# Optimization experiments

Hardware: AMD Instinct MI355X
Metric: run time of the kernel (lower is better)

## Reference

```python
import jax, jax.numpy as jnp
import numpy as np

IN_CH, OUT_CH, HIDDEN, NUM_BASIS = 256, 2, 8, 8
B, H, W = 16, 160, 160


def setup_inputs() -> dict:
    key = jax.random.key(0)
    k_x, k_cw, k_cb, k_ow = jax.random.split(key, 4)
    x = jax.random.normal(k_x, (B, IN_CH, H, W), dtype=jnp.float32)
    # 1x1 conv params (kaiming-ish scale)
    conv_w = jax.random.normal(k_cw, (HIDDEN, IN_CH), dtype=jnp.float32) / np.sqrt(IN_CH)
    conv_b = jax.random.normal(k_cb, (HIDDEN,), dtype=jnp.float32) * 0.01
    # RBF centers: linspace(-1.5, 1.5, num_basis) repeated over hidden
    base = jnp.linspace(-1.5, 1.5, NUM_BASIS, dtype=jnp.float32)
    centers = jnp.broadcast_to(base.reshape(1, 1, NUM_BASIS, 1, 1), (1, HIDDEN, NUM_BASIS, 1, 1)).astype(jnp.float32)
    log_widths = jnp.full((1, HIDDEN, NUM_BASIS, 1, 1), -0.2, dtype=jnp.float32)
    out_weight = jax.random.normal(k_ow, (OUT_CH, HIDDEN, NUM_BASIS), dtype=jnp.float32) * 0.03
    out_bias = jnp.zeros((OUT_CH,), dtype=jnp.float32)
    return {"x": x, "conv_w": conv_w, "conv_b": conv_b, "centers": centers,
            "log_widths": log_widths, "out_weight": out_weight, "out_bias": out_bias}


def reference(x, conv_w, conv_b, centers, log_widths, out_weight, out_bias):
    # 1x1 conv: [B,C,H,W] x [hidden,C] -> [B,hidden,H,W]
    z = jnp.einsum('bchw,kc->bkhw', x, conv_w) + conv_b[None, :, None, None]
    z = z[:, :, None, :, :]                       # [B,hidden,1,H,W]
    widths = jax.nn.softplus(log_widths) + 0.001  # [1,hidden,num_basis,1,1]
    phi = jnp.exp(-jnp.square((z - centers) / widths))  # [B,hidden,num_basis,H,W]
    out = jnp.einsum('bckhw,ock->bohw', phi, out_weight)
    return out + out_bias[None, :, None, None]
```

## Files before the change

kernel.cpp:

```cpp
#include <hip/hip_runtime.h>
#include <math.h>

#define IN_CH   256
#define HIDDEN  8
#define NBASIS  8
#define OUT_CH  2
#define HWD     25600
#define BATCH   16
#define PPT     4

__global__ __launch_bounds__(256) void rbf_fused_kernel(
    const float* __restrict__ x,
    const float* __restrict__ conv_w,
    const float* __restrict__ conv_b,
    const float* __restrict__ centers,
    const float* __restrict__ log_widths,
    const float* __restrict__ out_w,
    const float* __restrict__ out_bias,
    float* __restrict__ out)
{
    __shared__ float s_w[IN_CH][HIDDEN];
    __shared__ float s_cen[HIDDEN * NBASIS];
    __shared__ float s_iw[HIDDEN * NBASIS];
    __shared__ float s_ow0[HIDDEN * NBASIS];
    __shared__ float s_ow1[HIDDEN * NBASIS];
    __shared__ float s_cb[HIDDEN];
    __shared__ float s_ob[OUT_CH];

    const int tid = threadIdx.x;

    for (int i = tid; i < IN_CH * HIDDEN; i += 256) {
        const int c = i >> 3, k = i & 7;
        s_w[c][k] = conv_w[k * IN_CH + c];
    }
    if (tid < HIDDEN * NBASIS) {
        s_cen[tid] = centers[tid];
        const float wdt = log1pf(__expf(log_widths[tid])) + 0.001f;
        s_iw[tid]  = 1.0f / wdt;
        s_ow0[tid] = out_w[tid];
        s_ow1[tid] = out_w[HIDDEN * NBASIS + tid];
    }
    if (tid < HIDDEN) s_cb[tid] = conv_b[tid];
    if (tid < OUT_CH) s_ob[tid] = out_bias[tid];
    __syncthreads();

    const long long g  = (long long)blockIdx.x * 256 + tid;
    const long long p0 = g * PPT;
    const int b  = (int)(p0 / HWD);
    const int hw = (int)(p0 % HWD);
    const float* xp = x + (long long)b * IN_CH * HWD + hw;

    float acc[HIDDEN][PPT];
    #pragma unroll
    for (int k = 0; k < HIDDEN; ++k) {
        const float cb = s_cb[k];
        acc[k][0] = cb; acc[k][1] = cb; acc[k][2] = cb; acc[k][3] = cb;
    }

    #pragma unroll 8
    for (int c = 0; c < IN_CH; ++c) {
        const float4 xv = *reinterpret_cast<const float4*>(xp + (long long)c * HWD);
        #pragma unroll
        for (int k = 0; k < HIDDEN; ++k) {
            const float w = s_w[c][k];
            acc[k][0] = fmaf(xv.x, w, acc[k][0]);
            acc[k][1] = fmaf(xv.y, w, acc[k][1]);
            acc[k][2] = fmaf(xv.z, w, acc[k][2]);
            acc[k][3] = fmaf(xv.w, w, acc[k][3]);
        }
    }

    float o0[PPT], o1[PPT];
    #pragma unroll
    for (int p = 0; p < PPT; ++p) { o0[p] = s_ob[0]; o1[p] = s_ob[1]; }

    #pragma unroll
    for (int k = 0; k < HIDDEN; ++k) {
        #pragma unroll
        for (int j = 0; j < NBASIS; ++j) {
            const int   kj  = k * NBASIS + j;
            const float cen = s_cen[kj];
            const float iw  = s_iw[kj];
            const float w0  = s_ow0[kj];
            const float w1  = s_ow1[kj];
            #pragma unroll
            for (int p = 0; p < PPT; ++p) {
                const float t   = (acc[k][p] - cen) * iw;
                const float phi = __expf(-t * t);
                o0[p] = fmaf(phi, w0, o0[p]);
                o1[p] = fmaf(phi, w1, o1[p]);
            }
        }
    }

    float* op0 = out + ((long long)b * OUT_CH + 0) * HWD + hw;
    float* op1 = out + ((long long)b * OUT_CH + 1) * HWD + hw;
    *reinterpret_cast<float4*>(op0) = make_float4(o0[0], o0[1], o0[2], o0[3]);
    *reinterpret_cast<float4*>(op1) = make_float4(o1[0], o1[1], o1[2], o1[3]);
}

extern "C" void kernel_launch(void* const* d_in, const int* in_sizes, int n_in,
                              void* d_out, int out_size, void* d_ws, size_t ws_size,
                              hipStream_t stream) {
    const float* x          = (const float*)d_in[0];
    const float* conv_w     = (const float*)d_in[1];
    const float* conv_b     = (const float*)d_in[2];
    const float* centers    = (const float*)d_in[3];
    const float* log_widths = (const float*)d_in[4];
    const float* out_w      = (const float*)d_in[5];
    const float* out_bias   = (const float*)d_in[6];
    float* out = (float*)d_out;

    const int groups = BATCH * HWD / PPT;
    const int blocks = groups / 256;
    rbf_fused_kernel<<<blocks, 256, 0, stream>>>(
        x, conv_w, conv_b, centers, log_widths, out_w, out_bias, out);
}
```

Measured before the change: 610.9 us.

## Halve pixels per thread and add register prefetch ring for input channels

```diff
diff --git a/kernel.cpp b/kernel.cpp
--- a/kernel.cpp
+++ b/kernel.cpp
@@ -7,7 +7,8 @@
 #define OUT_CH  2
 #define HWD     25600
 #define BATCH   16
-#define PPT     4
+#define PPT     2
+#define PF      8
 
 __global__ __launch_bounds__(256) void rbf_fused_kernel(
     const float* __restrict__ x,
@@ -44,29 +45,58 @@
     if (tid < OUT_CH) s_ob[tid] = out_bias[tid];
     __syncthreads();
 
-    const long long g  = (long long)blockIdx.x * 256 + tid;
-    const long long p0 = g * PPT;
-    const int b  = (int)(p0 / HWD);
-    const int hw = (int)(p0 % HWD);
-    const float* xp = x + (long long)b * IN_CH * HWD + hw;
+    const int g  = blockIdx.x * 256 + tid;
+    const int p0 = g * PPT;
+    const int b  = p0 / HWD;
+    const int hw = p0 % HWD;
+    const float* xp = x + b * (IN_CH * HWD) + hw;
 
     float acc[HIDDEN][PPT];
     #pragma unroll
     for (int k = 0; k < HIDDEN; ++k) {
         const float cb = s_cb[k];
-        acc[k][0] = cb; acc[k][1] = cb; acc[k][2] = cb; acc[k][3] = cb;
+        acc[k][0] = cb; acc[k][1] = cb;
     }
 
-    #pragma unroll 8
-    for (int c = 0; c < IN_CH; ++c) {
-        const float4 xv = *reinterpret_cast<const float4*>(xp + (long long)c * HWD);
+    float2 buf[PF];
+    #pragma unroll
+    for (int j = 0; j < PF; ++j)
+        buf[j] = *reinterpret_cast<const float2*>(xp + j * HWD);
+
+    for (int c0 = 0; c0 < IN_CH - PF; c0 += PF) {
         #pragma unroll
-        for (int k = 0; k < HIDDEN; ++k) {
-            const float w = s_w[c][k];
-            acc[k][0] = fmaf(xv.x, w, acc[k][0]);
-            acc[k][1] = fmaf(xv.y, w, acc[k][1]);
-            acc[k][2] = fmaf(xv.z, w, acc[k][2]);
-            acc[k][3] = fmaf(xv.w, w, acc[k][3]);
+        for (int j = 0; j < PF; ++j) {
+            const float2 xv = buf[j];
+            buf[j] = *reinterpret_cast<const float2*>(xp + (c0 + PF + j) * HWD);
+            const int c = c0 + j;
+            const float4 wlo = *reinterpret_cast<const float4*>(&s_w[c][0]);
+            const float4 whi = *reinterpret_cast<const float4*>(&s_w[c][4]);
+            acc[0][0] = fmaf(xv.x, wlo.x, acc[0][0]); acc[0][1] = fmaf(xv.y, wlo.x, acc[0][1]);
+            acc[1][0] = fmaf(xv.x, wlo.y, acc[1][0]); acc[1][1] = fmaf(xv.y, wlo.y, acc[1][1]);
+            acc[2][0] = fmaf(xv.x, wlo.z, acc[2][0]); acc[2][1] = fmaf(xv.y, wlo.z, acc[2][1]);
+            acc[3][0] = fmaf(xv.x, wlo.w, acc[3][0]); acc[3][1] = fmaf(xv.y, wlo.w, acc[3][1]);
+            acc[4][0] = fmaf(xv.x, whi.x, acc[4][0]); acc[4][1] = fmaf(xv.y, whi.x, acc[4][1]);
+            acc[5][0] = fmaf(xv.x, whi.y, acc[5][0]); acc[5][1] = fmaf(xv.y, whi.y, acc[5][1]);
+            acc[6][0] = fmaf(xv.x, whi.z, acc[6][0]); acc[6][1] = fmaf(xv.y, whi.z, acc[6][1]);
+            acc[7][0] = fmaf(xv.x, whi.w, acc[7][0]); acc[7][1] = fmaf(xv.y, whi.w, acc[7][1]);
+        }
+    }
+    {
+        const int c0 = IN_CH - PF;
+        #pragma unroll
+        for (int j = 0; j < PF; ++j) {
+            const float2 xv = buf[j];
+            const int c = c0 + j;
+            const float4 wlo = *reinterpret_cast<const float4*>(&s_w[c][0]);
+            const float4 whi = *reinterpret_cast<const float4*>(&s_w[c][4]);
+            acc[0][0] = fmaf(xv.x, wlo.x, acc[0][0]); acc[0][1] = fmaf(xv.y, wlo.x, acc[0][1]);
+            acc[1][0] = fmaf(xv.x, wlo.y, acc[1][0]); acc[1][1] = fmaf(xv.y, wlo.y, acc[1][1]);
+            acc[2][0] = fmaf(xv.x, wlo.z, acc[2][0]); acc[2][1] = fmaf(xv.y, wlo.z, acc[2][1]);
+            acc[3][0] = fmaf(xv.x, wlo.w, acc[3][0]); acc[3][1] = fmaf(xv.y, wlo.w, acc[3][1]);
+            acc[4][0] = fmaf(xv.x, whi.x, acc[4][0]); acc[4][1] = fmaf(xv.y, whi.x, acc[4][1]);
+            acc[5][0] = fmaf(xv.x, whi.y, acc[5][0]); acc[5][1] = fmaf(xv.y, whi.y, acc[5][1]);
+            acc[6][0] = fmaf(xv.x, whi.z, acc[6][0]); acc[6][1] = fmaf(xv.y, whi.z, acc[6][1]);
+            acc[7][0] = fmaf(xv.x, whi.w, acc[7][0]); acc[7][1] = fmaf(xv.y, whi.w, acc[7][1]);
         }
     }
 
@@ -93,10 +123,10 @@
         }
     }
 
-    float* op0 = out + ((long long)b * OUT_CH + 0) * HWD + hw;
-    float* op1 = out + ((long long)b * OUT_CH + 1) * HWD + hw;
-    *reinterpret_cast<float4*>(op0) = make_float4(o0[0], o0[1], o0[2], o0[3]);
-    *reinterpret_cast<float4*>(op1) = make_float4(o1[0], o1[1], o1[2], o1[3]);
+    float* op0 = out + (b * OUT_CH + 0) * HWD + hw;
+    float* op1 = out + (b * OUT_CH + 1) * HWD + hw;
+    *reinterpret_cast<float2*>(op0) = make_float2(o0[0], o0[1]);
+    *reinterpret_cast<float2*>(op1) = make_float2(o1[0], o1[1]);
 }
 
 extern "C" void kernel_launch(void* const* d_in, const int* in_sizes, int n_in,
```

Result: faster. 563.9 us (-7.7%).

## Stream input channels through double-buffered LDS via async global_load_lds

Applied to the files above, without the earlier changes.

```diff
diff --git a/kernel.cpp b/kernel.cpp
--- a/kernel.cpp
+++ b/kernel.cpp
@@ -1,13 +1,15 @@
 #include <hip/hip_runtime.h>
 #include <math.h>
 
-#define IN_CH   256
-#define HIDDEN  8
-#define NBASIS  8
-#define OUT_CH  2
-#define HWD     25600
-#define BATCH   16
-#define PPT     4
+#define IN_CH    256
+#define HIDDEN   8
+#define NBASIS   8
+#define OUT_CH   2
+#define HWD      25600
+#define BATCH    16
+#define PXB      256
+#define CH_CHUNK 8
+#define NCHUNK   (IN_CH / CH_CHUNK)
 
 __global__ __launch_bounds__(256) void rbf_fused_kernel(
     const float* __restrict__ x,
@@ -19,6 +21,7 @@
     const float* __restrict__ out_bias,
     float* __restrict__ out)
 {
+    __shared__ float tile[2][CH_CHUNK][PXB];
     __shared__ float s_w[IN_CH][HIDDEN];
     __shared__ float s_cen[HIDDEN * NBASIS];
     __shared__ float s_iw[HIDDEN * NBASIS];
@@ -27,7 +30,9 @@
     __shared__ float s_cb[HIDDEN];
     __shared__ float s_ob[OUT_CH];
 
-    const int tid = threadIdx.x;
+    const int tid  = threadIdx.x;
+    const int wv   = tid >> 6;
+    const int lane = tid & 63;
 
     for (int i = tid; i < IN_CH * HIDDEN; i += 256) {
         const int c = i >> 3, k = i & 7;
@@ -42,61 +47,71 @@
     }
     if (tid < HIDDEN) s_cb[tid] = conv_b[tid];
     if (tid < OUT_CH) s_ob[tid] = out_bias[tid];
+
+    const int img = blockIdx.x / (HWD / PXB);
+    const int hw0 = (blockIdx.x % (HWD / PXB)) * PXB;
+    const float* xbase = x + img * (IN_CH * HWD) + hw0;
+
+    auto stage = [&](int cc, int bf) {
+        const int c0 = cc * CH_CHUNK;
+        #pragma unroll
+        for (int rr = 0; rr < 2; ++rr) {
+            const int r = wv + rr * 4;
+            const float* gp = xbase + (c0 + r) * HWD + lane * 4;
+            __builtin_amdgcn_global_load_lds(
+                (const __attribute__((address_space(1))) void*)gp,
+                (__attribute__((address_space(3))) void*)&tile[bf][r][0],
+                16, 0, 0);
+        }
+    };
+
+    float acc[HIDDEN];
+
+    stage(0, 0);
     __syncthreads();
 
-    const long long g  = (long long)blockIdx.x * 256 + tid;
-    const long long p0 = g * PPT;
-    const int b  = (int)(p0 / HWD);
-    const int hw = (int)(p0 % HWD);
-    const float* xp = x + (long long)b * IN_CH * HWD + hw;
+    #pragma unroll
+    for (int k = 0; k < HIDDEN; ++k) acc[k] = s_cb[k];
 
-    float acc[HIDDEN][PPT];
+    int bf = 0;
+    for (int cc = 0; cc < NCHUNK; ++cc) {
+        if (cc + 1 < NCHUNK) stage(cc + 1, bf ^ 1);
+        const int c0 = cc * CH_CHUNK;
+        #pragma unroll
+        for (int r = 0; r < CH_CHUNK; ++r) {
+            const float xv = tile[bf][r][tid];
+            const int c = c0 + r;
+            const float4 wlo = *reinterpret_cast<const float4*>(&s_w[c][0]);
+            const float4 whi = *reinterpret_cast<const float4*>(&s_w[c][4]);
+            acc[0] = fmaf(xv, wlo.x, acc[0]);
+            acc[1] = fmaf(xv, wlo.y, acc[1]);
+            acc[2] = fmaf(xv, wlo.z, acc[2]);
+            acc[3] = fmaf(xv, wlo.w, acc[3]);
+            acc[4] = fmaf(xv, whi.x, acc[4]);
+            acc[5] = fmaf(xv, whi.y, acc[5]);
+            acc[6] = fmaf(xv, whi.z, acc[6]);
+            acc[7] = fmaf(xv, whi.w, acc[7]);
+        }
+        __syncthreads();
+        bf ^= 1;
+    }
+
+    float o0 = s_ob[0], o1 = s_ob[1];
     #pragma unroll
     for (int k = 0; k < HIDDEN; ++k) {
-        const float cb = s_cb[k];
-        acc[k][0] = cb; acc[k][1] = cb; acc[k][2] = cb; acc[k][3] = cb;
-    }
-
-    #pragma unroll 8
-    for (int c = 0; c < IN_CH; ++c) {
-        const float4 xv = *reinterpret_cast<const float4*>(xp + (long long)c * HWD);
+        const float z = acc[k];
         #pragma unroll
-        for (int k = 0; k < HIDDEN; ++k) {
-            const float w = s_w[c][k];
-            acc[k][0] = fmaf(xv.x, w, acc[k][0]);
-            acc[k][1] = fmaf(xv.y, w, acc[k][1]);
-            acc[k][2] = fmaf(xv.z, w, acc[k][2]);
-            acc[k][3] = fmaf(xv.w, w, acc[k][3]);
+        for (int j = 0; j < NBASIS; ++j) {
+            const int kj = k * NBASIS + j;
+            const float t   = (z - s_cen[kj]) * s_iw[kj];
+            const float phi = __expf(-t * t);
+            o0 = fmaf(phi, s_ow0[kj], o0);
+            o1 = fmaf(phi, s_ow1[kj], o1);
         }
     }
 
-    float o0[PPT], o1[PPT];
-    #pragma unroll
-    for (int p = 0; p < PPT; ++p) { o0[p] = s_ob[0]; o1[p] = s_ob[1]; }
-
-    #pragma unroll
-    for (int k = 0; k < HIDDEN; ++k) {
-        #pragma unroll
-        for (int j = 0; j < NBASIS; ++j) {
-            const int   kj  = k * NBASIS + j;
-            const float cen = s_cen[kj];
-            const float iw  = s_iw[kj];
-            const float w0  = s_ow0[kj];
-            const float w1  = s_ow1[kj];
-            #pragma unroll
-            for (int p = 0; p < PPT; ++p) {
-                const float t   = (acc[k][p] - cen) * iw;
-                const float phi = __expf(-t * t);
-                o0[p] = fmaf(phi, w0, o0[p]);
-                o1[p] = fmaf(phi, w1, o1[p]);
-            }
-        }
-    }
-
-    float* op0 = out + ((long long)b * OUT_CH + 0) * HWD + hw;
-    float* op1 = out + ((long long)b * OUT_CH + 1) * HWD + hw;
-    *reinterpret_cast<float4*>(op0) = make_float4(o0[0], o0[1], o0[2], o0[3]);
-    *reinterpret_cast<float4*>(op1) = make_float4(o1[0], o1[1], o1[2], o1[3]);
+    out[(img * OUT_CH + 0) * HWD + hw0 + tid] = o0;
+    out[(img * OUT_CH + 1) * HWD + hw0 + tid] = o1;
 }
 
 extern "C" void kernel_launch(void* const* d_in, const int* in_sizes, int n_in,
@@ -111,8 +126,7 @@
     const float* out_bias   = (const float*)d_in[6];
     float* out = (float*)d_out;
 
-    const int groups = BATCH * HWD / PPT;
-    const int blocks = groups / 256;
+    const int blocks = BATCH * (HWD / PXB);
     rbf_fused_kernel<<<blocks, 256, 0, stream>>>(
         x, conv_w, conv_b, centers, log_widths, out_w, out_bias, out);
 }
```

New measurement: 572.6 us. -6.3%, faster.
